# Kernel tuning notes

Measured on AMD Instinct MI355X. Metric: run time of the kernel, lower is better.

## Reference

```python
import jax, jax.numpy as jnp
import numpy as np

INV_DELTA = 15.0  # inv_delta init kwarg


def setup_inputs() -> dict:
    key = jax.random.key(0)
    k1, k2 = jax.random.split(key)
    features = jax.random.normal(k1, (64, 1024, 14, 14), dtype=jnp.float32)
    # torch init: randn(num_words, num_channels).clamp(min=0)
    embedding = jnp.clip(jax.random.normal(k2, (8192, 1024), dtype=jnp.float32), 0.0, None)
    min_distance_mean = jnp.ones((1,), dtype=jnp.float32) * 0.5  # buffer init
    return {"features": features, "embedding": embedding,
            "min_distance_mean": min_distance_mean}


def reference(features, embedding, min_distance_mean):
    # BoWExtractor.forward in eval mode (no dictionary queue update / EMA).
    f = features[:, :, 1:-1, 1:-1]                      # [B,C,12,12] crop border
    emb_sq = jnp.sum(embedding * embedding, axis=1)     # [K]  ||w_k||^2
    cross = jnp.einsum('bchw,kc->bkhw', f, embedding)   # 1x1 conv == GEMM
    # squared L2 distance to every codeword: [B,K,12,12]
    dist = jnp.sum(f * f, axis=1, keepdims=True) - 2.0 * cross \
           + emb_sq[None, :, None, None]
    inv_delta_adaptive = INV_DELTA / min_distance_mean[0]
    codes = jax.nn.softmax(-inv_delta_adaptive * dist, axis=1)  # soft assignment over K
    bow = jnp.max(codes, axis=(2, 3))                   # global max-pool -> [B,K]
    bow = bow / jnp.sum(jnp.abs(bow), axis=1, keepdims=True)  # L1 normalize
    return bow, codes
```

## Files before the change

kernel.cpp:

```cpp
#include <hip/hip_runtime.h>
#include <math.h>

#define BB   64
#define CC   1024
#define HWC  144
#define KK   8192
#define MM   9216
#define NBN  128

typedef __attribute__((ext_vector_type(8)))  short          bf16x8;
typedef __attribute__((ext_vector_type(8)))  unsigned short u16x8;
typedef __attribute__((ext_vector_type(4)))  float          f32x4;
typedef __attribute__((ext_vector_type(16))) float          f32x16;

#define FA_BYTES  ((size_t)MM * CC * 2 * 2)
#define FB_BYTES  ((size_t)KK * CC * 2 * 2)
#define OFF_FA    0
#define OFF_FB    (OFF_FA + FA_BYTES)
#define OFF_ESQ   (OFF_FB + FB_BYTES)
#define OFF_PM    (OFF_ESQ + (size_t)KK * 4)
#define OFF_PS    (OFF_PM + (size_t)NBN * MM * 4)
#define OFF_FACT  (OFF_PS + (size_t)NBN * MM * 4)

__device__ inline unsigned short f2bf(float x) {
    union { float f; unsigned u; } v; v.f = x;
    unsigned r = v.u + 0x7fffu + ((v.u >> 16) & 1u);
    return (unsigned short)(r >> 16);
}
__device__ inline float bf2f(unsigned short h) {
    union { unsigned u; float f; } v; v.u = (unsigned)h << 16;
    return v.f;
}

__global__ __launch_bounds__(256)
void prep_A(const float* __restrict__ feat, u16x8* __restrict__ fA) {
    __shared__ float tile[64][145];
    int cb = blockIdx.x;
    int b  = blockIdx.y;
    for (int idx = threadIdx.x; idx < 64 * 144; idx += 256) {
        int r = idx / 144, hw = idx - r * 144;
        int h = hw / 12, w = hw - h * 12;
        tile[r][hw] = feat[(size_t)((b * 1024 + cb * 64 + r) * 196)
                           + (h + 1) * 14 + (w + 1)];
    }
    __syncthreads();
    for (int idx = threadIdx.x; idx < 8 * 144; idx += 256) {
        int g = idx / 144, hw = idx - g * 144;
        int p = b * 144 + hw;
        int bm = p >> 8, row = p & 255;
        int c = cb * 64 + g * 8;
        int kt = c >> 4, oct = (c >> 3) & 1;
        u16x8 hi, lo;
#pragma unroll
        for (int e = 0; e < 8; ++e) {
            float x = tile[g * 8 + e][hw];
            unsigned short h16 = f2bf(x);
            hi[e] = (short)h16;
            lo[e] = (short)f2bf(x - bf2f(h16));
        }
        size_t base = ((size_t)bm * 64 + kt) * 1024 + oct * 256 + row;
        fA[base] = hi;
        fA[base + 512] = lo;
    }
}

__global__ __launch_bounds__(256)
void prep_B(const float* __restrict__ emb, u16x8* __restrict__ fB) {
    __shared__ float tile[128][65];
    int cb = blockIdx.x;
    int nb = blockIdx.y;
#pragma unroll
    for (int i = 0; i < 8; ++i) {
        int idx = threadIdx.x + i * 256;
        int nl = idx >> 4, c4 = idx & 15;
        const float4 v = *reinterpret_cast<const float4*>(
            emb + (size_t)(nb * 128 + nl) * 1024 + cb * 64 + c4 * 4);
        tile[nl][c4 * 4 + 0] = v.x;
        tile[nl][c4 * 4 + 1] = v.y;
        tile[nl][c4 * 4 + 2] = v.z;
        tile[nl][c4 * 4 + 3] = v.w;
    }
    __syncthreads();
#pragma unroll
    for (int i = 0; i < 4; ++i) {
        int idx = threadIdx.x + i * 256;
        int kc = idx >> 7, rl = idx & 127;
        int c = cb * 64 + kc * 8;
        int kt = c >> 4, oct = (c >> 3) & 1;
        u16x8 hi, lo;
#pragma unroll
        for (int e = 0; e < 8; ++e) {
            float x = tile[rl][kc * 8 + e];
            unsigned short h16 = f2bf(x);
            hi[e] = (short)h16;
            lo[e] = (short)f2bf(x - bf2f(h16));
        }
        size_t base = ((size_t)nb * 64 + kt) * 512 + oct * 128 + rl;
        fB[base] = hi;
        fB[base + 256] = lo;
    }
}

__global__ void rowsumsq(const float* __restrict__ src, float* __restrict__ dst) {
    int row = blockIdx.x * 4 + (threadIdx.x >> 6);
    int l = threadIdx.x & 63;
    const float4* p = reinterpret_cast<const float4*>(src + (size_t)row * 1024);
    float s = 0.f;
#pragma unroll
    for (int it = 0; it < 4; ++it) {
        float4 v = p[l + it * 64];
        s += v.x * v.x + v.y * v.y + v.z * v.z + v.w * v.w;
    }
#pragma unroll
    for (int off = 32; off; off >>= 1) s += __shfl_down(s, off);
    if (l == 0) dst[row] = s;
}

__global__ __launch_bounds__(256, 2)
void gemm_mfma(const char* __restrict__ fA, const char* __restrict__ fB,
               const float* __restrict__ esq, const float* __restrict__ mdm,
               float* __restrict__ codes, float* __restrict__ pm,
               float* __restrict__ ps) {
    __shared__ __align__(16) char smem[49152];

    int flat = blockIdx.x;
    int swz = (flat & 7) * 288 + (flat >> 3);
    int bm = swz >> 6, bn = swz & 63;

    int tid = threadIdx.x;
    int l = tid & 63, l31 = l & 31, lc2 = l >> 5;
    int wv = tid >> 6, wr = wv >> 1, wc = wv & 1;

    const char* gA = fA + (size_t)bm * 1048576;
    const char* gB = fB + (size_t)bn * 524288;

    f32x16 acc[4][2];
#pragma unroll
    for (int i = 0; i < 4; ++i)
#pragma unroll
        for (int j = 0; j < 2; ++j)
#pragma unroll
            for (int r = 0; r < 16; ++r) acc[i][j][r] = 0.f;

    auto stage = [&](int buf, int kt) {
        char* db = smem + buf * 24576;
        const char* ga = gA + (size_t)kt * 16384;
        const char* gb = gB + (size_t)kt * 8192;
#pragma unroll
        for (int i = 0; i < 4; ++i) {
            int off = i * 4096 + tid * 16;
            __builtin_amdgcn_global_load_lds(
                (const __attribute__((address_space(1))) void*)(ga + off),
                (__attribute__((address_space(3))) void*)(db + off), 16, 0, 0);
        }
#pragma unroll
        for (int i = 0; i < 2; ++i) {
            int off = i * 4096 + tid * 16;
            __builtin_amdgcn_global_load_lds(
                (const __attribute__((address_space(1))) void*)(gb + off),
                (__attribute__((address_space(3))) void*)(db + 16384 + off), 16, 0, 0);
        }
    };

    stage(0, 0);
    stage(1, 1);

    for (int kt = 0; kt < 64; ++kt) {
        asm volatile("s_waitcnt vmcnt(6)" ::: "memory");
        __builtin_amdgcn_s_barrier();
        __builtin_amdgcn_sched_barrier(0);

        const char* bufc = smem + (kt & 1) * 24576;
        bf16x8 ah[4], al[4], bh[2], bl[2];
#pragma unroll
        for (int f = 0; f < 4; ++f) {
            int ao = (lc2 * 256 + wr * 128 + f * 32 + l31) * 16;
            ah[f] = *(const bf16x8*)(bufc + ao);
            al[f] = *(const bf16x8*)(bufc + 8192 + ao);
        }
#pragma unroll
        for (int f = 0; f < 2; ++f) {
            int bo = 16384 + (lc2 * 128 + wc * 64 + f * 32 + l31) * 16;
            bh[f] = *(const bf16x8*)(bufc + bo);
            bl[f] = *(const bf16x8*)(bufc + 4096 + bo);
        }
        __builtin_amdgcn_s_setprio(1);
#pragma unroll
        for (int fi = 0; fi < 4; ++fi)
#pragma unroll
            for (int fj = 0; fj < 2; ++fj) {
                f32x16& A = acc[fi][fj];
                A = __builtin_amdgcn_mfma_f32_32x32x16_bf16(ah[fi], bh[fj], A, 0, 0, 0);
                A = __builtin_amdgcn_mfma_f32_32x32x16_bf16(ah[fi], bl[fj], A, 0, 0, 0);
                A = __builtin_amdgcn_mfma_f32_32x32x16_bf16(al[fi], bh[fj], A, 0, 0, 0);
            }
        __builtin_amdgcn_s_setprio(0);
        __builtin_amdgcn_s_barrier();
        int kn = (kt + 2 > 63) ? 63 : kt + 2;
        stage(kt & 1, kn);
    }

    float invl2 = (15.0f / mdm[0]) * 1.44269504089f;
    float s2 = 2.0f * invl2;
    float e2[2];
#pragma unroll
    for (int fj = 0; fj < 2; ++fj)
        e2[fj] = invl2 * esq[bn * 128 + wc * 64 + fj * 32 + l31];

    int bnp = bn * 2 + wc;

#pragma unroll
    for (int fi = 0; fi < 4; ++fi) {
        float mx[16], ss[16];
#pragma unroll
        for (int fj = 0; fj < 2; ++fj)
#pragma unroll
            for (int r = 0; r < 16; ++r)
                acc[fi][fj][r] = s2 * acc[fi][fj][r] - e2[fj];
#pragma unroll
        for (int r = 0; r < 16; ++r)
            mx[r] = fmaxf(acc[fi][0][r], acc[fi][1][r]);
#pragma unroll
        for (int off = 1; off < 32; off <<= 1)
#pragma unroll
            for (int r = 0; r < 16; ++r)
                mx[r] = fmaxf(mx[r], __shfl_xor(mx[r], off));
#pragma unroll
        for (int r = 0; r < 16; ++r) ss[r] = 0.f;
#pragma unroll
        for (int fj = 0; fj < 2; ++fj)
#pragma unroll
            for (int r = 0; r < 16; ++r) {
                float E = exp2f(acc[fi][fj][r] - mx[r]);
                acc[fi][fj][r] = E;
                ss[r] += E;
            }
#pragma unroll
        for (int off = 1; off < 32; off <<= 1)
#pragma unroll
            for (int r = 0; r < 16; ++r)
                ss[r] += __shfl_xor(ss[r], off);

        if (l31 == 0) {
#pragma unroll
            for (int r = 0; r < 16; ++r) {
                int row = wr * 128 + fi * 32 + 8 * (r >> 2) + 4 * lc2 + (r & 3);
                int p = bm * 256 + row;
                pm[(size_t)bnp * MM + p] = mx[r];
                ps[(size_t)bnp * MM + p] = ss[r];
            }
        }

#pragma unroll
        for (int fj = 0; fj < 2; ++fj) {
            int k = bn * 128 + wc * 64 + fj * 32 + l31;
#pragma unroll
            for (int q = 0; q < 4; ++q) {
                int p0 = bm * 256 + wr * 128 + fi * 32 + 8 * q + 4 * lc2;
                int b = p0 / 144, hw = p0 - b * 144;
                f32x4 v;
                v.x = acc[fi][fj][q * 4 + 0];
                v.y = acc[fi][fj][q * 4 + 1];
                v.z = acc[fi][fj][q * 4 + 2];
                v.w = acc[fi][fj][q * 4 + 3];
                __builtin_nontemporal_store(
                    v, (f32x4*)(codes + ((size_t)(b * 8192 + k)) * 144 + hw));
            }
        }
    }
}

__global__ void comb_factor(const float* __restrict__ pm,
                            const float* __restrict__ ps,
                            float* __restrict__ factor) {
    int p = blockIdx.x * 256 + threadIdx.x;
    float m = -INFINITY;
#pragma unroll 8
    for (int bn = 0; bn < NBN; ++bn) m = fmaxf(m, pm[(size_t)bn * MM + p]);
    float S = 0.f;
#pragma unroll 8
    for (int bn = 0; bn < NBN; ++bn)
        S += ps[(size_t)bn * MM + p] * exp2f(pm[(size_t)bn * MM + p] - m);
    float is = 1.f / S;
#pragma unroll 8
    for (int bn = 0; bn < NBN; ++bn)
        factor[(size_t)bn * MM + p] = exp2f(pm[(size_t)bn * MM + p] - m) * is;
}

__global__ __launch_bounds__(256)
void scale_bow(float* __restrict__ codes, const float* __restrict__ factor,
               float* __restrict__ bow) {
    int wid = threadIdx.x >> 6, l = threadIdx.x & 63;
    int r = blockIdx.x * 4 + wid;
    int b = r >> 13, k = r & 8191;
    f32x4* Cp = (f32x4*)(codes + (size_t)r * 144);
    const f32x4* Fp = (const f32x4*)(factor + (size_t)(k >> 6) * MM + b * 144);
    float m = 0.f;
    if (l < 36) {
        f32x4 e = __builtin_nontemporal_load(Cp + l);
        f32x4 f = Fp[l];
        f32x4 v = e * f;
        __builtin_nontemporal_store(v, Cp + l);
        m = fmaxf(fmaxf(v.x, v.y), fmaxf(v.z, v.w));
    }
#pragma unroll
    for (int off = 32; off; off >>= 1) m = fmaxf(m, __shfl_down(m, off));
    if (l == 0) bow[r] = m;
}

__global__ void bow_norm(float* __restrict__ bow) {
    __shared__ float lds[4];
    __shared__ float stot;
    int b = blockIdx.x;
    float* p = bow + b * 8192;
    float s = 0.f;
    for (int i = threadIdx.x; i < 8192; i += 256) s += fabsf(p[i]);
#pragma unroll
    for (int off = 32; off; off >>= 1) s += __shfl_down(s, off);
    int wid = threadIdx.x >> 6, l = threadIdx.x & 63;
    if (l == 0) lds[wid] = s;
    __syncthreads();
    if (threadIdx.x == 0) stot = 1.f / (lds[0] + lds[1] + lds[2] + lds[3]);
    __syncthreads();
    float inv = stot;
    for (int i = threadIdx.x; i < 8192; i += 256) p[i] *= inv;
}

extern "C" void kernel_launch(void* const* d_in, const int* in_sizes, int n_in,
                              void* d_out, int out_size, void* d_ws, size_t ws_size,
                              hipStream_t stream) {
    const float* feat = (const float*)d_in[0];
    const float* emb  = (const float*)d_in[1];
    const float* mdm  = (const float*)d_in[2];
    float* bow   = (float*)d_out;
    float* codes = (float*)d_out + (size_t)BB * KK;

    char* ws = (char*)d_ws;
    u16x8* fA    = (u16x8*)(ws + OFF_FA);
    u16x8* fB    = (u16x8*)(ws + OFF_FB);
    float* esq   = (float*)(ws + OFF_ESQ);
    float* pm    = (float*)(ws + OFF_PM);
    float* ps    = (float*)(ws + OFF_PS);
    float* fact  = (float*)(ws + OFF_FACT);

    prep_A<<<dim3(16, 64), 256, 0, stream>>>(feat, fA);
    prep_B<<<dim3(16, 64), 256, 0, stream>>>(emb, fB);
    rowsumsq<<<KK / 4, 256, 0, stream>>>(emb, esq);
    gemm_mfma<<<2304, 256, 0, stream>>>((const char*)fA, (const char*)fB,
                                        esq, mdm, codes, pm, ps);
    comb_factor<<<36, 256, 0, stream>>>(pm, ps, fact);
    scale_bow<<<(BB * KK) / 4, 256, 0, stream>>>(codes, fact, bow);
    bow_norm<<<BB, 256, 0, stream>>>(bow);
}
```

Baseline: 644.8 us.

## Store intermediate exp values as bf16 and triple-buffer GEMM LDS stages

The GEMM epilogue can now write the unnormalized softmax numerators as bf16 into a workspace buffer instead of fp32 into the codes output. The scaling kernel then reads bf16 and writes fp32 codes, which cuts the intermediate round-trip traffic roughly in half. Separately, the GEMM main loop moves from double to triple buffering in LDS (72KB) with a deeper prefetch. This adds bf16 rounding error to the codes, and the larger LDS use may lower occupancy. The bf16 path only runs when the workspace is large enough.

```diff
diff --git a/kernel.cpp b/kernel.cpp
--- a/kernel.cpp
+++ b/kernel.cpp
@@ -10,6 +10,7 @@
 
 typedef __attribute__((ext_vector_type(8)))  short          bf16x8;
 typedef __attribute__((ext_vector_type(8)))  unsigned short u16x8;
+typedef __attribute__((ext_vector_type(4)))  unsigned short u16x4;
 typedef __attribute__((ext_vector_type(4)))  float          f32x4;
 typedef __attribute__((ext_vector_type(16))) float          f32x16;
 
@@ -21,6 +22,9 @@
 #define OFF_PM    (OFF_ESQ + (size_t)KK * 4)
 #define OFF_PS    (OFF_PM + (size_t)NBN * MM * 4)
 #define OFF_FACT  (OFF_PS + (size_t)NBN * MM * 4)
+#define OFF_E     (OFF_FACT + (size_t)NBN * MM * 4)
+#define E_BYTES   ((size_t)BB * KK * HWC * 2)
+#define WS_NEED_B16 (OFF_E + E_BYTES)
 
 __device__ inline unsigned short f2bf(float x) {
     union { float f; unsigned u; } v; v.f = x;
@@ -120,8 +124,9 @@
 void gemm_mfma(const char* __restrict__ fA, const char* __restrict__ fB,
                const float* __restrict__ esq, const float* __restrict__ mdm,
                float* __restrict__ codes, float* __restrict__ pm,
-               float* __restrict__ ps) {
-    __shared__ __align__(16) char smem[49152];
+               float* __restrict__ ps, unsigned short* __restrict__ Ebf,
+               int ebf16) {
+    __shared__ __align__(16) char smem[73728];
 
     int flat = blockIdx.x;
     int swz = (flat & 7) * 288 + (flat >> 3);
@@ -164,13 +169,15 @@
 
     stage(0, 0);
     stage(1, 1);
-
+    stage(2, 2);
+
+    int cur = 0;
     for (int kt = 0; kt < 64; ++kt) {
-        asm volatile("s_waitcnt vmcnt(6)" ::: "memory");
+        asm volatile("s_waitcnt vmcnt(12)" ::: "memory");
         __builtin_amdgcn_s_barrier();
         __builtin_amdgcn_sched_barrier(0);
 
-        const char* bufc = smem + (kt & 1) * 24576;
+        const char* bufc = smem + cur * 24576;
         bf16x8 ah[4], al[4], bh[2], bl[2];
 #pragma unroll
         for (int f = 0; f < 4; ++f) {
@@ -196,9 +203,11 @@
             }
         __builtin_amdgcn_s_setprio(0);
         __builtin_amdgcn_s_barrier();
-        int kn = (kt + 2 > 63) ? 63 : kt + 2;
-        stage(kt & 1, kn);
-    }
+        int kn = (kt + 3 > 63) ? 63 : kt + 3;
+        stage(cur, kn);
+        cur = (cur == 2) ? 0 : cur + 1;
+    }
+    asm volatile("s_waitcnt vmcnt(0)" ::: "memory");
 
     float invl2 = (15.0f / mdm[0]) * 1.44269504089f;
     float s2 = 2.0f * invl2;
@@ -251,20 +260,39 @@
             }
         }
 
-#pragma unroll
-        for (int fj = 0; fj < 2; ++fj) {
-            int k = bn * 128 + wc * 64 + fj * 32 + l31;
-#pragma unroll
-            for (int q = 0; q < 4; ++q) {
-                int p0 = bm * 256 + wr * 128 + fi * 32 + 8 * q + 4 * lc2;
-                int b = p0 / 144, hw = p0 - b * 144;
-                f32x4 v;
-                v.x = acc[fi][fj][q * 4 + 0];
-                v.y = acc[fi][fj][q * 4 + 1];
-                v.z = acc[fi][fj][q * 4 + 2];
-                v.w = acc[fi][fj][q * 4 + 3];
-                __builtin_nontemporal_store(
-                    v, (f32x4*)(codes + ((size_t)(b * 8192 + k)) * 144 + hw));
+        if (ebf16) {
+#pragma unroll
+            for (int fj = 0; fj < 2; ++fj) {
+                int k = bn * 128 + wc * 64 + fj * 32 + l31;
+#pragma unroll
+                for (int q = 0; q < 4; ++q) {
+                    int p0 = bm * 256 + wr * 128 + fi * 32 + 8 * q + 4 * lc2;
+                    int b = p0 / 144, hw = p0 - b * 144;
+                    u16x4 v;
+                    v.x = f2bf(acc[fi][fj][q * 4 + 0]);
+                    v.y = f2bf(acc[fi][fj][q * 4 + 1]);
+                    v.z = f2bf(acc[fi][fj][q * 4 + 2]);
+                    v.w = f2bf(acc[fi][fj][q * 4 + 3]);
+                    __builtin_nontemporal_store(
+                        v, (u16x4*)(Ebf + ((size_t)(b * 8192 + k)) * 144 + hw));
+                }
+            }
+        } else {
+#pragma unroll
+            for (int fj = 0; fj < 2; ++fj) {
+                int k = bn * 128 + wc * 64 + fj * 32 + l31;
+#pragma unroll
+                for (int q = 0; q < 4; ++q) {
+                    int p0 = bm * 256 + wr * 128 + fi * 32 + 8 * q + 4 * lc2;
+                    int b = p0 / 144, hw = p0 - b * 144;
+                    f32x4 v;
+                    v.x = acc[fi][fj][q * 4 + 0];
+                    v.y = acc[fi][fj][q * 4 + 1];
+                    v.z = acc[fi][fj][q * 4 + 2];
+                    v.w = acc[fi][fj][q * 4 + 3];
+                    __builtin_nontemporal_store(
+                        v, (f32x4*)(codes + ((size_t)(b * 8192 + k)) * 144 + hw));
+                }
             }
         }
     }
@@ -288,8 +316,35 @@
 }
 
 __global__ __launch_bounds__(256)
-void scale_bow(float* __restrict__ codes, const float* __restrict__ factor,
-               float* __restrict__ bow) {
+void scale_bow_b16(const unsigned short* __restrict__ E,
+                   const float* __restrict__ factor,
+                   float* __restrict__ codes, float* __restrict__ bow) {
+    int wid = threadIdx.x >> 6, l = threadIdx.x & 63;
+    int r = blockIdx.x * 4 + wid;
+    int b = r >> 13, k = r & 8191;
+    const u16x4* Ep = (const u16x4*)(E + (size_t)r * 144);
+    f32x4* Cp = (f32x4*)(codes + (size_t)r * 144);
+    const f32x4* Fp = (const f32x4*)(factor + (size_t)(k >> 6) * MM + b * 144);
+    float m = 0.f;
+    if (l < 36) {
+        u16x4 e = __builtin_nontemporal_load(Ep + l);
+        f32x4 f = Fp[l];
+        f32x4 v;
+        v.x = bf2f(e.x) * f.x;
+        v.y = bf2f(e.y) * f.y;
+        v.z = bf2f(e.z) * f.z;
+        v.w = bf2f(e.w) * f.w;
+        __builtin_nontemporal_store(v, Cp + l);
+        m = fmaxf(fmaxf(v.x, v.y), fmaxf(v.z, v.w));
+    }
+#pragma unroll
+    for (int off = 32; off; off >>= 1) m = fmaxf(m, __shfl_down(m, off));
+    if (l == 0) bow[r] = m;
+}
+
+__global__ __launch_bounds__(256)
+void scale_bow_f32(float* __restrict__ codes, const float* __restrict__ factor,
+                   float* __restrict__ bow) {
     int wid = threadIdx.x >> 6, l = threadIdx.x & 63;
     int r = blockIdx.x * 4 + wid;
     int b = r >> 13, k = r & 8191;
@@ -342,13 +397,19 @@
     float* pm    = (float*)(ws + OFF_PM);
     float* ps    = (float*)(ws + OFF_PS);
     float* fact  = (float*)(ws + OFF_FACT);
+    unsigned short* Ebf = (unsigned short*)(ws + OFF_E);
+
+    int use_b16 = (ws_size >= WS_NEED_B16) ? 1 : 0;
 
     prep_A<<<dim3(16, 64), 256, 0, stream>>>(feat, fA);
     prep_B<<<dim3(16, 64), 256, 0, stream>>>(emb, fB);
     rowsumsq<<<KK / 4, 256, 0, stream>>>(emb, esq);
     gemm_mfma<<<2304, 256, 0, stream>>>((const char*)fA, (const char*)fB,
-                                        esq, mdm, codes, pm, ps);
+                                        esq, mdm, codes, pm, ps, Ebf, use_b16);
     comb_factor<<<36, 256, 0, stream>>>(pm, ps, fact);
-    scale_bow<<<(BB * KK) / 4, 256, 0, stream>>>(codes, fact, bow);
+    if (use_b16)
+        scale_bow_b16<<<(BB * KK) / 4, 256, 0, stream>>>(Ebf, fact, codes, bow);
+    else
+        scale_bow_f32<<<(BB * KK) / 4, 256, 0, stream>>>(codes, fact, bow);
     bow_norm<<<BB, 256, 0, stream>>>(bow);
 }
```

After: 654.9 us. No clear change (+1.6%).

## Use single bf16 GEMM and refine significant softmax entries in fp32

Applied to the files above, without the earlier changes.

Drops the split-bf16 (hi/lo) 3-MFMA scheme, so the main GEMM runs one bf16 MFMA per tile and half the operand bytes. The exponent tile is stored as bf16 instead of fp32, and the softmax statistics are combined across column blocks. Entries whose provisional probability exceeds a threshold are collected into a capped list and recomputed with exact fp32 dot products. The softmax max and sum are then corrected with these values and scattered back into codes and bow. This trades GEMM precision and bandwidth for several extra small kernels, atomics and a precision risk if the candidate count overflows the cap.

```diff
diff --git a/kernel.cpp b/kernel.cpp
--- a/kernel.cpp
+++ b/kernel.cpp
@@ -7,20 +7,31 @@
 #define KK   8192
 #define MM   9216
 #define NBN  128
+#define CAP  2000000
+#define THR  1e-9f
 
 typedef __attribute__((ext_vector_type(8)))  short          bf16x8;
 typedef __attribute__((ext_vector_type(8)))  unsigned short u16x8;
+typedef __attribute__((ext_vector_type(4)))  unsigned short u16x4;
 typedef __attribute__((ext_vector_type(4)))  float          f32x4;
 typedef __attribute__((ext_vector_type(16))) float          f32x16;
 
-#define FA_BYTES  ((size_t)MM * CC * 2 * 2)
-#define FB_BYTES  ((size_t)KK * CC * 2 * 2)
 #define OFF_FA    0
-#define OFF_FB    (OFF_FA + FA_BYTES)
-#define OFF_ESQ   (OFF_FB + FB_BYTES)
+#define OFF_FB    (OFF_FA + (size_t)MM * CC * 2)
+#define OFF_ESQ   (OFF_FB + (size_t)KK * CC * 2)
 #define OFF_PM    (OFF_ESQ + (size_t)KK * 4)
 #define OFF_PS    (OFF_PM + (size_t)NBN * MM * 4)
 #define OFF_FACT  (OFF_PS + (size_t)NBN * MM * 4)
+#define OFF_MA    (OFF_FACT + (size_t)NBN * MM * 4)
+#define OFF_SA    (OFF_MA + (size_t)MM * 4)
+#define OFF_SSUB  (OFF_SA + (size_t)MM * 4)
+#define OFF_M2U   (OFF_SSUB + (size_t)MM * 4)
+#define OFF_SCAND (OFF_M2U + (size_t)MM * 4)
+#define OFF_ISTOT (OFF_SCAND + (size_t)MM * 4)
+#define OFF_CNT   (OFF_ISTOT + (size_t)MM * 4)
+#define OFF_CPOS  (OFF_CNT + 64)
+#define OFF_CL2   (OFF_CPOS + (size_t)CAP * 4)
+#define OFF_E     (OFF_CL2 + (size_t)CAP * 4)
 
 __device__ inline unsigned short f2bf(float x) {
     union { float f; unsigned u; } v; v.f = x;
@@ -30,6 +41,21 @@
 __device__ inline float bf2f(unsigned short h) {
     union { unsigned u; float f; } v; v.u = (unsigned)h << 16;
     return v.f;
+}
+__device__ inline unsigned ordOf(float x) {
+    unsigned u = __float_as_uint(x);
+    return (x >= 0.f) ? (u | 0x80000000u) : ~u;
+}
+__device__ inline float ordToF(unsigned o) {
+    return (o & 0x80000000u) ? __uint_as_float(o & 0x7fffffffu)
+                             : __uint_as_float(~o);
+}
+
+__global__ void init_aux(float* S_sub, unsigned* m2u, float* Scand,
+                         unsigned* cnt) {
+    int i = blockIdx.x * 256 + threadIdx.x;
+    if (i < MM) { S_sub[i] = 0.f; m2u[i] = 0u; Scand[i] = 0.f; }
+    if (i == 0) cnt[0] = 0u;
 }
 
 __global__ __launch_bounds__(256)
@@ -50,17 +76,10 @@
         int bm = p >> 8, row = p & 255;
         int c = cb * 64 + g * 8;
         int kt = c >> 4, oct = (c >> 3) & 1;
-        u16x8 hi, lo;
-#pragma unroll
-        for (int e = 0; e < 8; ++e) {
-            float x = tile[g * 8 + e][hw];
-            unsigned short h16 = f2bf(x);
-            hi[e] = (short)h16;
-            lo[e] = (short)f2bf(x - bf2f(h16));
-        }
-        size_t base = ((size_t)bm * 64 + kt) * 1024 + oct * 256 + row;
-        fA[base] = hi;
-        fA[base + 512] = lo;
+        u16x8 hi;
+#pragma unroll
+        for (int e = 0; e < 8; ++e) hi[e] = f2bf(tile[g * 8 + e][hw]);
+        fA[((size_t)bm * 64 + kt) * 512 + oct * 256 + row] = hi;
     }
 }
 
@@ -87,17 +106,10 @@
         int kc = idx >> 7, rl = idx & 127;
         int c = cb * 64 + kc * 8;
         int kt = c >> 4, oct = (c >> 3) & 1;
-        u16x8 hi, lo;
-#pragma unroll
-        for (int e = 0; e < 8; ++e) {
-            float x = tile[rl][kc * 8 + e];
-            unsigned short h16 = f2bf(x);
-            hi[e] = (short)h16;
-            lo[e] = (short)f2bf(x - bf2f(h16));
-        }
-        size_t base = ((size_t)nb * 64 + kt) * 512 + oct * 128 + rl;
-        fB[base] = hi;
-        fB[base + 256] = lo;
+        u16x8 hi;
+#pragma unroll
+        for (int e = 0; e < 8; ++e) hi[e] = f2bf(tile[rl][kc * 8 + e]);
+        fB[((size_t)nb * 64 + kt) * 256 + oct * 128 + rl] = hi;
     }
 }
 
@@ -117,10 +129,10 @@
 }
 
 __global__ __launch_bounds__(256, 2)
-void gemm_mfma(const char* __restrict__ fA, const char* __restrict__ fB,
-               const float* __restrict__ esq, const float* __restrict__ mdm,
-               float* __restrict__ codes, float* __restrict__ pm,
-               float* __restrict__ ps) {
+void gemm1(const char* __restrict__ fA, const char* __restrict__ fB,
+           const float* __restrict__ esq, const float* __restrict__ mdm,
+           float* __restrict__ pm, float* __restrict__ ps,
+           unsigned short* __restrict__ Ebf) {
     __shared__ __align__(16) char smem[49152];
 
     int flat = blockIdx.x;
@@ -131,8 +143,8 @@
     int l = tid & 63, l31 = l & 31, lc2 = l >> 5;
     int wv = tid >> 6, wr = wv >> 1, wc = wv & 1;
 
-    const char* gA = fA + (size_t)bm * 1048576;
-    const char* gB = fB + (size_t)bn * 524288;
+    const char* gA = fA + (size_t)bm * 524288;
+    const char* gB = fB + (size_t)bn * 262144;
 
     f32x16 acc[4][2];
 #pragma unroll
@@ -142,62 +154,56 @@
 #pragma unroll
             for (int r = 0; r < 16; ++r) acc[i][j][r] = 0.f;
 
-    auto stage = [&](int buf, int kt) {
+    auto stage = [&](int buf, int t) {
+        int ts = t > 31 ? 31 : t;
         char* db = smem + buf * 24576;
-        const char* ga = gA + (size_t)kt * 16384;
-        const char* gb = gB + (size_t)kt * 8192;
-#pragma unroll
-        for (int i = 0; i < 4; ++i) {
-            int off = i * 4096 + tid * 16;
+        const char* ga = gA + (size_t)ts * 16384;
+        const char* gb = gB + (size_t)ts * 8192;
+#pragma unroll
+        for (int c = 0; c < 4; ++c) {
             __builtin_amdgcn_global_load_lds(
-                (const __attribute__((address_space(1))) void*)(ga + off),
-                (__attribute__((address_space(3))) void*)(db + off), 16, 0, 0);
-        }
-#pragma unroll
-        for (int i = 0; i < 2; ++i) {
-            int off = i * 4096 + tid * 16;
+                (const __attribute__((address_space(1))) void*)(ga + c * 4096 + tid * 16),
+                (__attribute__((address_space(3))) void*)(db + c * 4096 + tid * 16), 16, 0, 0);
+        }
+#pragma unroll
+        for (int c = 0; c < 2; ++c) {
             __builtin_amdgcn_global_load_lds(
-                (const __attribute__((address_space(1))) void*)(gb + off),
-                (__attribute__((address_space(3))) void*)(db + 16384 + off), 16, 0, 0);
+                (const __attribute__((address_space(1))) void*)(gb + c * 4096 + tid * 16),
+                (__attribute__((address_space(3))) void*)(db + 16384 + c * 4096 + tid * 16), 16, 0, 0);
         }
     };
 
     stage(0, 0);
     stage(1, 1);
 
-    for (int kt = 0; kt < 64; ++kt) {
+    for (int t = 0; t < 32; ++t) {
         asm volatile("s_waitcnt vmcnt(6)" ::: "memory");
         __builtin_amdgcn_s_barrier();
         __builtin_amdgcn_sched_barrier(0);
 
-        const char* bufc = smem + (kt & 1) * 24576;
-        bf16x8 ah[4], al[4], bh[2], bl[2];
-#pragma unroll
-        for (int f = 0; f < 4; ++f) {
-            int ao = (lc2 * 256 + wr * 128 + f * 32 + l31) * 16;
-            ah[f] = *(const bf16x8*)(bufc + ao);
-            al[f] = *(const bf16x8*)(bufc + 8192 + ao);
-        }
-#pragma unroll
-        for (int f = 0; f < 2; ++f) {
-            int bo = 16384 + (lc2 * 128 + wc * 64 + f * 32 + l31) * 16;
-            bh[f] = *(const bf16x8*)(bufc + bo);
-            bl[f] = *(const bf16x8*)(bufc + 4096 + bo);
-        }
-        __builtin_amdgcn_s_setprio(1);
-#pragma unroll
-        for (int fi = 0; fi < 4; ++fi)
-#pragma unroll
-            for (int fj = 0; fj < 2; ++fj) {
-                f32x16& A = acc[fi][fj];
-                A = __builtin_amdgcn_mfma_f32_32x32x16_bf16(ah[fi], bh[fj], A, 0, 0, 0);
-                A = __builtin_amdgcn_mfma_f32_32x32x16_bf16(ah[fi], bl[fj], A, 0, 0, 0);
-                A = __builtin_amdgcn_mfma_f32_32x32x16_bf16(al[fi], bh[fj], A, 0, 0, 0);
-            }
-        __builtin_amdgcn_s_setprio(0);
+        const char* bufc = smem + (t & 1) * 24576;
+#pragma unroll
+        for (int kt2 = 0; kt2 < 2; ++kt2) {
+            bf16x8 ah[4], bh[2];
+#pragma unroll
+            for (int f = 0; f < 4; ++f)
+                ah[f] = *(const bf16x8*)(bufc + kt2 * 8192 + lc2 * 4096
+                                         + (wr * 128 + f * 32 + l31) * 16);
+#pragma unroll
+            for (int f = 0; f < 2; ++f)
+                bh[f] = *(const bf16x8*)(bufc + 16384 + kt2 * 4096 + lc2 * 2048
+                                         + (wc * 64 + f * 32 + l31) * 16);
+            __builtin_amdgcn_s_setprio(1);
+#pragma unroll
+            for (int fi = 0; fi < 4; ++fi)
+#pragma unroll
+                for (int fj = 0; fj < 2; ++fj)
+                    acc[fi][fj] = __builtin_amdgcn_mfma_f32_32x32x16_bf16(
+                        ah[fi], bh[fj], acc[fi][fj], 0, 0, 0);
+            __builtin_amdgcn_s_setprio(0);
+        }
         __builtin_amdgcn_s_barrier();
-        int kn = (kt + 2 > 63) ? 63 : kt + 2;
-        stage(kt & 1, kn);
+        stage(t & 1, t + 2);
     }
 
     float invl2 = (15.0f / mdm[0]) * 1.44269504089f;
@@ -250,7 +256,6 @@
                 ps[(size_t)bnp * MM + p] = ss[r];
             }
         }
-
 #pragma unroll
         for (int fj = 0; fj < 2; ++fj) {
             int k = bn * 128 + wc * 64 + fj * 32 + l31;
@@ -258,21 +263,21 @@
             for (int q = 0; q < 4; ++q) {
                 int p0 = bm * 256 + wr * 128 + fi * 32 + 8 * q + 4 * lc2;
                 int b = p0 / 144, hw = p0 - b * 144;
-                f32x4 v;
-                v.x = acc[fi][fj][q * 4 + 0];
-                v.y = acc[fi][fj][q * 4 + 1];
-                v.z = acc[fi][fj][q * 4 + 2];
-                v.w = acc[fi][fj][q * 4 + 3];
+                u16x4 v;
+                v.x = f2bf(acc[fi][fj][q * 4 + 0]);
+                v.y = f2bf(acc[fi][fj][q * 4 + 1]);
+                v.z = f2bf(acc[fi][fj][q * 4 + 2]);
+                v.w = f2bf(acc[fi][fj][q * 4 + 3]);
                 __builtin_nontemporal_store(
-                    v, (f32x4*)(codes + ((size_t)(b * 8192 + k)) * 144 + hw));
+                    v, (u16x4*)(Ebf + ((size_t)(b * 8192 + k)) * 144 + hw));
             }
         }
     }
 }
 
-__global__ void comb_factor(const float* __restrict__ pm,
-                            const float* __restrict__ ps,
-                            float* __restrict__ factor) {
+__global__ void comb1(const float* __restrict__ pm, const float* __restrict__ ps,
+                      float* __restrict__ fact, float* __restrict__ m_a,
+                      float* __restrict__ S_a) {
     int p = blockIdx.x * 256 + threadIdx.x;
     float m = -INFINITY;
 #pragma unroll 8
@@ -284,28 +289,156 @@
     float is = 1.f / S;
 #pragma unroll 8
     for (int bn = 0; bn < NBN; ++bn)
-        factor[(size_t)bn * MM + p] = exp2f(pm[(size_t)bn * MM + p] - m) * is;
+        fact[(size_t)bn * MM + p] = exp2f(pm[(size_t)bn * MM + p] - m) * is;
+    m_a[p] = m;
+    S_a[p] = S;
 }
 
 __global__ __launch_bounds__(256)
-void scale_bow(float* __restrict__ codes, const float* __restrict__ factor,
-               float* __restrict__ bow) {
+void detect(unsigned short* __restrict__ E, const float* __restrict__ fact,
+            const float* __restrict__ pm, float* __restrict__ S_sub,
+            unsigned* __restrict__ cnt, int* __restrict__ cpos) {
     int wid = threadIdx.x >> 6, l = threadIdx.x & 63;
     int r = blockIdx.x * 4 + wid;
     int b = r >> 13, k = r & 8191;
+    u16x4* Ep = (u16x4*)(E + (size_t)r * 144);
+    const float* Fr = fact + (size_t)(k >> 6) * MM + b * 144;
+    const float* Pr = pm + (size_t)(k >> 6) * MM + b * 144;
+    if (l < 36) {
+        u16x4 e = Ep[l];
+        f32x4 f = *(const f32x4*)(Fr + l * 4);
+        bool mod = false;
+#pragma unroll
+        for (int j = 0; j < 4; ++j) {
+            float Ef = bf2f(e[j]);
+            float v = Ef * f[j];
+            if (v > THR) {
+                int hw = l * 4 + j;
+                int p = b * 144 + hw;
+                unsigned idx = atomicAdd(cnt, 1u);
+                if (idx < CAP) {
+                    cpos[idx] = r * 144 + hw;
+                    atomicAdd(&S_sub[p], v);
+                    e[j] = 0;
+                    mod = true;
+                }
+            }
+        }
+        if (mod) Ep[l] = e;
+    }
+}
+
+__global__ __launch_bounds__(256)
+void refine1(const int* __restrict__ cpos, const unsigned* __restrict__ cnt,
+             const float* __restrict__ feat, const float* __restrict__ emb,
+             const float* __restrict__ esq, const float* __restrict__ mdm,
+             float* __restrict__ cl2, unsigned* __restrict__ m2u) {
+    int l = threadIdx.x & 63;
+    int gw = blockIdx.x * 4 + (threadIdx.x >> 6);
+    int nw = gridDim.x * 4;
+    int n = (int)min(cnt[0], (unsigned)CAP);
+    float invl2 = (15.0f / mdm[0]) * 1.44269504089f;
+    for (int i = gw; i < n; i += nw) {
+        int pos = cpos[i];
+        int r = pos / 144, hw = pos - r * 144;
+        int b = r >> 13, k = r & 8191;
+        int h = hw / 12, w = hw - h * 12;
+        int c0 = l * 16;
+        const float* fp = feat + ((size_t)(b * 1024 + c0)) * 196
+                          + (h + 1) * 14 + (w + 1);
+        const float4* ep = (const float4*)(emb + (size_t)k * 1024 + c0);
+        float dot = 0.f;
+#pragma unroll
+        for (int j4 = 0; j4 < 4; ++j4) {
+            float4 ev = ep[j4];
+            dot = fmaf(fp[(size_t)(j4 * 4 + 0) * 196], ev.x, dot);
+            dot = fmaf(fp[(size_t)(j4 * 4 + 1) * 196], ev.y, dot);
+            dot = fmaf(fp[(size_t)(j4 * 4 + 2) * 196], ev.z, dot);
+            dot = fmaf(fp[(size_t)(j4 * 4 + 3) * 196], ev.w, dot);
+        }
+#pragma unroll
+        for (int off = 32; off; off >>= 1) dot += __shfl_xor(dot, off);
+        if (l == 0) {
+            float l2 = invl2 * (2.f * dot - esq[k]);
+            cl2[i] = l2;
+            int p = b * 144 + hw;
+            atomicMax(&m2u[p], ordOf(l2));
+        }
+    }
+}
+
+__global__ void refine2(const int* __restrict__ cpos, const float* __restrict__ cl2,
+                        const unsigned* __restrict__ cnt,
+                        const unsigned* __restrict__ m2u,
+                        float* __restrict__ Scand) {
+    int gt = blockIdx.x * 256 + threadIdx.x;
+    int nt = gridDim.x * 256;
+    int n = (int)min(cnt[0], (unsigned)CAP);
+    for (int i = gt; i < n; i += nt) {
+        int pos = cpos[i];
+        int r = pos / 144, hw = pos - r * 144;
+        int p = (r >> 13) * 144 + hw;
+        atomicAdd(&Scand[p], exp2f(cl2[i] - ordToF(m2u[p])));
+    }
+}
+
+__global__ void comb2(const float* __restrict__ pm, const float* __restrict__ m_a,
+                      const float* __restrict__ S_a, const float* __restrict__ S_sub,
+                      const unsigned* __restrict__ m2u, const float* __restrict__ Scand,
+                      float* __restrict__ fact, float* __restrict__ iStot) {
+    int p = blockIdx.x * 256 + threadIdx.x;
+    float m2 = ordToF(m2u[p]);
+    float Snc = S_a[p] * fmaxf(1.f - S_sub[p], 0.f);
+    float Stot = Snc * exp2f(m_a[p] - m2) + Scand[p];
+    float inv = 1.f / Stot;
+    iStot[p] = inv;
+#pragma unroll 8
+    for (int bn = 0; bn < NBN; ++bn)
+        fact[(size_t)bn * MM + p] = exp2f(pm[(size_t)bn * MM + p] - m2) * inv;
+}
+
+__global__ __launch_bounds__(256)
+void scale_bow(const unsigned short* __restrict__ E, const float* __restrict__ fact,
+               float* __restrict__ codes, float* __restrict__ bow) {
+    int wid = threadIdx.x >> 6, l = threadIdx.x & 63;
+    int r = blockIdx.x * 4 + wid;
+    int b = r >> 13, k = r & 8191;
+    const u16x4* Ep = (const u16x4*)(E + (size_t)r * 144);
     f32x4* Cp = (f32x4*)(codes + (size_t)r * 144);
-    const f32x4* Fp = (const f32x4*)(factor + (size_t)(k >> 6) * MM + b * 144);
+    const f32x4* Fp = (const f32x4*)(fact + (size_t)(k >> 6) * MM + b * 144);
     float m = 0.f;
     if (l < 36) {
-        f32x4 e = __builtin_nontemporal_load(Cp + l);
+        u16x4 e = __builtin_nontemporal_load(Ep + l);
         f32x4 f = Fp[l];
-        f32x4 v = e * f;
+        f32x4 v;
+        v.x = bf2f(e.x) * f.x;
+        v.y = bf2f(e.y) * f.y;
+        v.z = bf2f(e.z) * f.z;
+        v.w = bf2f(e.w) * f.w;
         __builtin_nontemporal_store(v, Cp + l);
         m = fmaxf(fmaxf(v.x, v.y), fmaxf(v.z, v.w));
     }
 #pragma unroll
     for (int off = 32; off; off >>= 1) m = fmaxf(m, __shfl_down(m, off));
     if (l == 0) bow[r] = m;
+}
+
+__global__ void scatter(const int* __restrict__ cpos, const float* __restrict__ cl2,
+                        const unsigned* __restrict__ cnt,
+                        const unsigned* __restrict__ m2u,
+                        const float* __restrict__ iStot,
+                        float* __restrict__ codes, float* __restrict__ bow) {
+    int gt = blockIdx.x * 256 + threadIdx.x;
+    int nt = gridDim.x * 256;
+    int n = (int)min(cnt[0], (unsigned)CAP);
+    for (int i = gt; i < n; i += nt) {
+        int pos = cpos[i];
+        int r = pos / 144, hw = pos - r * 144;
+        int p = (r >> 13) * 144 + hw;
+        float v = exp2f(cl2[i] - ordToF(m2u[p])) * iStot[p];
+        codes[pos] = v;
+        atomicMax((unsigned*)&bow[r], __float_as_uint(v));
+    }
 }
 
 __global__ void bow_norm(float* __restrict__ bow) {
@@ -336,19 +469,35 @@
     float* codes = (float*)d_out + (size_t)BB * KK;
 
     char* ws = (char*)d_ws;
-    u16x8* fA    = (u16x8*)(ws + OFF_FA);
-    u16x8* fB    = (u16x8*)(ws + OFF_FB);
-    float* esq   = (float*)(ws + OFF_ESQ);
-    float* pm    = (float*)(ws + OFF_PM);
-    float* ps    = (float*)(ws + OFF_PS);
-    float* fact  = (float*)(ws + OFF_FACT);
-
+    u16x8* fA     = (u16x8*)(ws + OFF_FA);
+    u16x8* fB     = (u16x8*)(ws + OFF_FB);
+    float* esq    = (float*)(ws + OFF_ESQ);
+    float* pm     = (float*)(ws + OFF_PM);
+    float* ps     = (float*)(ws + OFF_PS);
+    float* fact   = (float*)(ws + OFF_FACT);
+    float* m_a    = (float*)(ws + OFF_MA);
+    float* S_a    = (float*)(ws + OFF_SA);
+    float* S_sub  = (float*)(ws + OFF_SSUB);
+    unsigned* m2u = (unsigned*)(ws + OFF_M2U);
+    float* Scand  = (float*)(ws + OFF_SCAND);
+    float* iStot  = (float*)(ws + OFF_ISTOT);
+    unsigned* cnt = (unsigned*)(ws + OFF_CNT);
+    int* cpos     = (int*)(ws + OFF_CPOS);
+    float* cl2    = (float*)(ws + OFF_CL2);
+    unsigned short* Ebf = (unsigned short*)(ws + OFF_E);
+
+    init_aux<<<36, 256, 0, stream>>>(S_sub, m2u, Scand, cnt);
     prep_A<<<dim3(16, 64), 256, 0, stream>>>(feat, fA);
     prep_B<<<dim3(16, 64), 256, 0, stream>>>(emb, fB);
     rowsumsq<<<KK / 4, 256, 0, stream>>>(emb, esq);
-    gemm_mfma<<<2304, 256, 0, stream>>>((const char*)fA, (const char*)fB,
-                                        esq, mdm, codes, pm, ps);
-    comb_factor<<<36, 256, 0, stream>>>(pm, ps, fact);
-    scale_bow<<<(BB * KK) / 4, 256, 0, stream>>>(codes, fact, bow);
+    gemm1<<<2304, 256, 0, stream>>>((const char*)fA, (const char*)fB,
+                                    esq, mdm, pm, ps, Ebf);
+    comb1<<<36, 256, 0, stream>>>(pm, ps, fact, m_a, S_a);
+    detect<<<(BB * KK) / 4, 256, 0, stream>>>(Ebf, fact, pm, S_sub, cnt, cpos);
+    refine1<<<1024, 256, 0, stream>>>(cpos, cnt, feat, emb, esq, mdm, cl2, m2u);
+    refine2<<<256, 256, 0, stream>>>(cpos, cl2, cnt, m2u, Scand);
+    comb2<<<36, 256, 0, stream>>>(pm, m_a, S_a, S_sub, m2u, Scand, fact, iStot);
+    scale_bow<<<(BB * KK) / 4, 256, 0, stream>>>(Ebf, fact, codes, bow);
+    scatter<<<256, 256, 0, stream>>>(cpos, cl2, cnt, m2u, iStot, codes, bow);
     bow_norm<<<BB, 256, 0, stream>>>(bow);
 }
```

After: 867.6 us. +34.6%, slower.
